# Optimization experiments

Measured on AMD Instinct MI355X. Metric: run time of the kernel, lower is better.

The kernel has to match this reference:

```python
import jax, jax.numpy as jnp
import numpy as np

H = 2048          # hidden_size
I = 8192          # intermediate_size (shared expert)
E = 32            # num_experts
K = 4             # num_experts_per_tok
M = 1408          # moe_intermediate_size
B, S = 2, 1024


def setup_inputs() -> dict:
    key = jax.random.key(0)
    ks = jax.random.split(key, 7)
    scale = 0.02
    return {
        "hidden_states": jax.random.normal(ks[0], (B, S, H), dtype=jnp.float32),
        "gate_w": jax.random.normal(ks[1], (H, E), dtype=jnp.float32) * scale,
        "w1": jax.random.normal(ks[2], (E, H, M), dtype=jnp.float32) * scale,  # expert up-proj
        "w2": jax.random.normal(ks[3], (E, M, H), dtype=jnp.float32) * scale,  # expert down-proj
        "ws1": jax.random.normal(ks[4], (H, I), dtype=jnp.float32) * scale,    # shared up-proj
        "ws2": jax.random.normal(ks[5], (I, H), dtype=jnp.float32) * scale,    # shared down-proj
    }


def reference(hidden_states, gate_w, w1, w2, ws1, ws2):
    b, s, h = hidden_states.shape
    x = hidden_states.reshape(-1, h)                      # [T, H]

    # shared expert: Linear -> SiLU -> Linear
    shared = jax.nn.silu(x @ ws1) @ ws2                   # [T, H]

    # router: top-k logits, softmax over the k selected logits
    router_logits = x @ gate_w                            # [T, E]
    top_vals, top_idx = jax.lax.top_k(router_logits, K)   # [T, K]
    routing_weights = jax.nn.softmax(top_vals, axis=-1)   # [T, K]

    # combine weights: scatter top-k weights into dense [T, E]
    cw = (jax.nn.one_hot(top_idx, E, dtype=x.dtype)
          * routing_weights[..., None]).sum(axis=1)       # [T, E]

    # expert FFNs (dense over experts, weighted combine)
    a = jax.nn.silu(jnp.einsum('th,ehm->tem', x, w1))     # [T, E, M]
    expert_out = jnp.einsum('tem,emh,te->th', a, w2, cw)  # [T, H]

    output = (shared + expert_out).reshape(b, s, h)
    return output, router_logits.reshape(b, s, E)
```

## Files before the change

kernel.cpp:

```cpp
#include <hip/hip_runtime.h>

#define H_ 2048
#define E_ 32
#define KSEL 4
#define M_ 1408
#define I_ 8192
#define T_ 2048

typedef __bf16 bf16;
typedef bf16 bf16x8 __attribute__((ext_vector_type(8)));
typedef float f32x4 __attribute__((ext_vector_type(4)));
typedef unsigned short u16x8 __attribute__((ext_vector_type(8)));
typedef unsigned int u32x4 __attribute__((ext_vector_type(4)));

static __device__ __forceinline__ unsigned short bfb(float f) {
  return __builtin_bit_cast(unsigned short, (bf16)f);
}

static __device__ __forceinline__ void gload_lds16(const void* g, void* l) {
  __builtin_amdgcn_global_load_lds((const __attribute__((address_space(1))) void*)g,
                                   (__attribute__((address_space(3))) void*)l, 16, 0, 0);
}

static __device__ __forceinline__ float silu_f(float v) {
  return v / (1.f + __expf(-v));
}

static __device__ __forceinline__ void wave_argmax(float& v, int& vi) {
  #pragma unroll
  for (int off = 32; off >= 1; off >>= 1) {
    float ov = __shfl_xor(v, off);
    int   oi = __shfl_xor(vi, off);
    if (ov > v || (ov == v && oi < vi)) { v = ov; vi = oi; }
  }
}

__global__ __launch_bounds__(64) void prep_k(int* __restrict__ counts) {
  if (threadIdx.x < E_) counts[threadIdx.x] = 0;
}

__global__ __launch_bounds__(256) void combine_k(const float* __restrict__ sc,
                                                 const float* __restrict__ sc2,
                                                 float* __restrict__ out) {
  size_t i = ((size_t)blockIdx.x * 256 + threadIdx.x) * 4;
  int t = (int)(i >> 11);
  int h = (int)(i & 2047);
  const float* s = sc + (size_t)(t * 4) * H_ + h;
  float4 a = *(const float4*)(s);
  float4 b = *(const float4*)(s + H_);
  float4 c = *(const float4*)(s + 2 * H_);
  float4 d = *(const float4*)(s + 3 * H_);
  float4 o;
  o.x = a.x + b.x + c.x + d.x;
  o.y = a.y + b.y + c.y + d.y;
  o.z = a.z + b.z + c.z + d.z;
  o.w = a.w + b.w + c.w + d.w;
  #pragma unroll
  for (int kz = 0; kz < 2; ++kz) {
    float4 v = *(const float4*)(sc2 + (size_t)kz * T_ * H_ + i);
    o.x += v.x; o.y += v.y; o.z += v.z; o.w += v.w;
  }
  *(float4*)(out + i) = o;
}

__global__ __launch_bounds__(64) void router_k(const float* __restrict__ x, const float* __restrict__ gw,
                                               float* __restrict__ logits, int* __restrict__ counts,
                                               int* __restrict__ tlist, float* __restrict__ wlist,
                                               unsigned short* __restrict__ xb) {
  int t = blockIdx.x;
  int l = threadIdx.x;

  {
    const float* xrow = x + (size_t)t * H_;
    unsigned short* xbrow = xb + (size_t)t * H_;
    #pragma unroll
    for (int j = 0; j < 4; ++j) {
      int base = j * 512 + l * 8;
      float4 a = *(const float4*)(xrow + base);
      float4 b = *(const float4*)(xrow + base + 4);
      u16x8 o;
      o[0]=bfb(a.x); o[1]=bfb(a.y); o[2]=bfb(a.z); o[3]=bfb(a.w);
      o[4]=bfb(b.x); o[5]=bfb(b.y); o[6]=bfb(b.z); o[7]=bfb(b.w);
      *(u16x8*)(xbrow + base) = o;
    }
  }

  int e = l & 31;
  int half = l >> 5;
  const float* xr = x + (size_t)t * H_ + half * (H_/2);
  const float* g  = gw + (size_t)(half * (H_/2)) * E_ + e;
  float a0=0.f, a1=0.f, a2=0.f, a3=0.f;
  for (int h = 0; h < H_/2; h += 4) {
    a0 = fmaf(xr[h],   g[(size_t)h*E_],     a0);
    a1 = fmaf(xr[h+1], g[(size_t)(h+1)*E_], a1);
    a2 = fmaf(xr[h+2], g[(size_t)(h+2)*E_], a2);
    a3 = fmaf(xr[h+3], g[(size_t)(h+3)*E_], a3);
  }
  float acc = (a0+a1)+(a2+a3);
  acc += __shfl_xor(acc, 32);
  if (l < E_) logits[(size_t)t*E_ + l] = acc;

  float cur = (l < E_) ? acc : -INFINITY;
  int myidx = (l < E_) ? e : 1000;
  float tv0,tv1,tv2,tv3; int ti0,ti1,ti2,ti3;
  { float v=cur; int vi=myidx; wave_argmax(v,vi); tv0=v; ti0=vi; if (myidx==vi) cur=-INFINITY; }
  { float v=cur; int vi=myidx; wave_argmax(v,vi); tv1=v; ti1=vi; if (myidx==vi) cur=-INFINITY; }
  { float v=cur; int vi=myidx; wave_argmax(v,vi); tv2=v; ti2=vi; if (myidx==vi) cur=-INFINITY; }
  { float v=cur; int vi=myidx; wave_argmax(v,vi); tv3=v; ti3=vi; }
  float w0 = 1.f;
  float w1 = __expf(tv1 - tv0);
  float w2 = __expf(tv2 - tv0);
  float w3 = __expf(tv3 - tv0);
  float inv = 1.f / (w0+w1+w2+w3);
  if (l < KSEL) {
    float myw = ((l==0)?w0:(l==1)?w1:(l==2)?w2:w3) * inv;
    int   myi = ((l==0)?ti0:(l==1)?ti1:(l==2)?ti2:ti3);
    int pos = atomicAdd(&counts[myi], 1);
    tlist[myi*T_ + pos] = (t << 2) | l;
    wlist[myi*T_ + pos] = myw;
  }
}

template<int MODE, int KDIM, int NDIM, int ASTR, int KSPLIT>
__device__ __forceinline__ void gemm_body(
    char* __restrict__ smem, int mt, int nt, int kz, int nrows,
    const bf16* __restrict__ A, const float* __restrict__ Bp,
    bf16* __restrict__ Cb, float* __restrict__ Cf,
    const int* __restrict__ lst, const float* __restrict__ wl)
{
  char* As = smem;
  char* Bs = smem + 16384;
  const int tid = threadIdx.x;
  const int mrow0 = mt*128, ncol0 = nt*64;

  const bf16* abase[4];
  int aoffs[4];
  #pragma unroll
  for (int c = 0; c < 4; ++c) {
    int lidx = c*256 + tid;
    int row  = lidx >> 3;
    int slot = lidx & 7;
    aoffs[c] = (slot ^ (row & 7)) * 8;
    int ri = mrow0 + row;
    if constexpr (MODE == 2) {
      int tt = (ri < nrows) ? (lst[ri] >> 2) : 0;
      abase[c] = A + (size_t)tt * ASTR;
    } else if constexpr (MODE == 3) {
      int ar = (ri < nrows) ? lst[ri] : 0;
      abase[c] = A + (size_t)ar * ASTR;
    } else {
      abase[c] = A + (size_t)ri * ASTR;
    }
  }

  const int bn = tid & 63;
  const int bq = tid >> 6;
  const float* bsrc0 = Bp + (size_t)(bq * 16) * NDIM + ncol0 + bn;
  char* const bdst = Bs + (bq*2)*1024 + bn*16;

  const int l  = tid & 63;
  const int wv = tid >> 6;
  const int wr = wv >> 1, wc = wv & 1;
  const int ss = l >> 4;

  f32x4 acc[4][2] = {};

  constexpr int ITERS = KDIM / 64 / KSPLIT;
  static_assert(ITERS % 2 == 0, "K-loop is 2-unrolled");
  const int kt0 = kz * ITERS;
  const int ktend = kt0 + ITERS;

  float vA[16], vB[16];

#define LOADB(P, KT) do {                                            \
    const float* bs_ = bsrc0 + (size_t)((KT) * 64) * NDIM;           \
    _Pragma("unroll")                                                \
    for (int j = 0; j < 16; ++j) P[j] = bs_[(size_t)j * NDIM];       \
  } while (0)

#define WRITEB(P) do {                                               \
    u32x4 lo_, hi_;                                                  \
    _Pragma("unroll")                                                \
    for (int j = 0; j < 4; ++j) {                                    \
      lo_[j] = (unsigned)bfb(P[2*j])   | ((unsigned)bfb(P[2*j+1]) << 16); \
      hi_[j] = (unsigned)bfb(P[8+2*j]) | ((unsigned)bfb(P[8+2*j+1]) << 16); \
    }                                                                \
    *(u32x4*)(bdst)        = lo_;                                    \
    *(u32x4*)(bdst + 1024) = hi_;                                    \
  } while (0)

#define MFMA_HALF(S) do {                                            \
    bf16x8 af[4], bfr[2];                                            \
    const int ks = (S)*4 + ss;                                       \
    _Pragma("unroll")                                                \
    for (int mf = 0; mf < 4; ++mf) {                                 \
      int r = wr*64 + mf*16 + (l & 15);                              \
      af[mf] = *(const bf16x8*)(As + r*128 + ((ks ^ (r & 7)) << 4)); \
    }                                                                \
    _Pragma("unroll")                                                \
    for (int nf = 0; nf < 2; ++nf) {                                 \
      int c = wc*32 + nf*16 + (l & 15);                              \
      bfr[nf] = *(const bf16x8*)(Bs + ks*1024 + c*16);               \
    }                                                                \
    _Pragma("unroll")                                                \
    for (int mf = 0; mf < 4; ++mf)                                   \
      _Pragma("unroll")                                              \
      for (int nf = 0; nf < 2; ++nf)                                 \
        acc[mf][nf] = __builtin_amdgcn_mfma_f32_16x16x32_bf16(af[mf], bfr[nf], acc[mf][nf], 0, 0, 0); \
  } while (0)

#define MFMA_PHASE() do { MFMA_HALF(0); MFMA_HALF(1); } while (0)

#define ADMA(KT) do {                                                \
    _Pragma("unroll")                                                \
    for (int c = 0; c < 4; ++c)                                      \
      gload_lds16(abase[c] + (KT)*64 + aoffs[c], As + (c*256 + tid)*16); \
  } while (0)

  LOADB(vA, kt0);
  for (int kt = kt0; kt < ktend; kt += 2) {
    __syncthreads();
    ADMA(kt);
    WRITEB(vA);
    __syncthreads();
    LOADB(vB, kt + 1);
    MFMA_PHASE();

    __syncthreads();
    ADMA(kt + 1);
    WRITEB(vB);
    __syncthreads();
    if (kt + 2 < ktend) LOADB(vA, kt + 2);
    MFMA_PHASE();
  }

#undef LOADB
#undef WRITEB
#undef MFMA_HALF
#undef MFMA_PHASE
#undef ADMA

  #pragma unroll
  for (int mf = 0; mf < 4; ++mf) {
    #pragma unroll
    for (int j = 0; j < 4; ++j) {
      const int rloc = wr*64 + mf*16 + (l >> 4)*4 + j;
      const int grow = mrow0 + rloc;
      if constexpr (MODE == 0) {
        #pragma unroll
        for (int nf = 0; nf < 2; ++nf) {
          int col = ncol0 + wc*32 + nf*16 + (l & 15);
          Cb[(size_t)grow * NDIM + col] = (bf16)silu_f(acc[mf][nf][j]);
        }
      } else if constexpr (MODE == 1) {
        float* dst = Cf + (size_t)kz * T_ * H_;
        #pragma unroll
        for (int nf = 0; nf < 2; ++nf) {
          int col = ncol0 + wc*32 + nf*16 + (l & 15);
          dst[(size_t)grow * NDIM + col] = acc[mf][nf][j];
        }
      } else if constexpr (MODE == 2) {
        if (grow < nrows) {
          int entry = lst[grow];
          float wg = wl[grow];
          #pragma unroll
          for (int nf = 0; nf < 2; ++nf) {
            int col = ncol0 + wc*32 + nf*16 + (l & 15);
            Cb[(size_t)entry * NDIM + col] = (bf16)(silu_f(acc[mf][nf][j]) * wg);
          }
        }
      } else {
        if (grow < nrows) {
          int entry = lst[grow];
          #pragma unroll
          for (int nf = 0; nf < 2; ++nf) {
            int col = ncol0 + wc*32 + nf*16 + (l & 15);
            Cf[(size_t)entry * H_ + col] = acc[mf][nf][j];
          }
        }
      }
    }
  }
}

__global__ __launch_bounds__(256) void fusedA_k(
    const bf16* __restrict__ xb, const float* __restrict__ w1, const float* __restrict__ ws1,
    bf16* __restrict__ act, bf16* __restrict__ y1,
    const int* __restrict__ tlist, const float* __restrict__ wlist, const int* __restrict__ counts)
{
  __shared__ __align__(16) char smem[24576];
  if (blockIdx.x < 1408) {
    constexpr int NT = M_ / 64;
    constexpr int NWG = NT * E_ * 2;
    constexpr int CPX = NWG / 8;
    int id = blockIdx.x;
    int lg = (id & 7) * CPX + (id >> 3);
    int bit = lg & 1;
    int en  = lg >> 1;
    int e  = en / NT;
    int nt = en % NT;
    int mt = (blockIdx.y == 0) ? bit : (2 + 2*((int)blockIdx.y - 1) + bit);
    int nrows = counts[e];
    if (mt * 128 >= nrows) return;
    gemm_body<2, 2048, M_, 2048, 1>(smem, mt, nt, 0, nrows,
        xb, w1 + (size_t)e * 2048 * M_, act, nullptr, tlist + e*T_, wlist + e*T_);
  } else {
    int t = ((int)blockIdx.x - 1408) * 8 + (int)blockIdx.y;
    constexpr int CPX = 2048 / 8;
    int lg = (t & 7) * CPX + (t >> 3);
    int mt = lg & 15;
    int nt = lg >> 4;
    gemm_body<0, 2048, I_, 2048, 1>(smem, mt, nt, 0, T_,
        xb, ws1, y1, nullptr, nullptr, nullptr);
  }
}

__global__ __launch_bounds__(256) void fusedB_k(
    const bf16* __restrict__ y1, const float* __restrict__ ws2,
    const bf16* __restrict__ act, const float* __restrict__ w2,
    float* __restrict__ scratch2, float* __restrict__ scratch,
    const int* __restrict__ tlist, const int* __restrict__ counts)
{
  __shared__ __align__(16) char smem[24576];
  if (blockIdx.x < 2048) {
    constexpr int NT = H_ / 64;
    constexpr int NWG = NT * E_ * 2;
    constexpr int CPX = NWG / 8;
    int id = blockIdx.x;
    int lg = (id & 7) * CPX + (id >> 3);
    int bit = lg & 1;
    int en  = lg >> 1;
    int e  = en / NT;
    int nt = en % NT;
    int mt = (blockIdx.y == 0) ? bit : (2 + 2*((int)blockIdx.y - 1) + bit);
    int nrows = counts[e];
    if (mt * 128 >= nrows) return;
    gemm_body<3, M_, H_, M_, 1>(smem, mt, nt, 0, nrows,
        act, w2 + (size_t)e * M_ * H_, nullptr, scratch, tlist + e*T_, nullptr);
  } else {
    int id = ((int)blockIdx.x - 2048) * 8 + (int)blockIdx.y;
    int kz  = id & 1;
    int sub = id >> 1;
    constexpr int CPX = 512 / 8;
    int lg = (sub & 7) * CPX + (sub >> 3);
    int mt = lg & 15;
    int nt = lg >> 4;
    gemm_body<1, I_, H_, I_, 2>(smem, mt, nt, kz, T_,
        y1, ws2, nullptr, scratch2, nullptr, nullptr);
  }
}

extern "C" void kernel_launch(void* const* d_in, const int* in_sizes, int n_in,
                              void* d_out, int out_size, void* d_ws, size_t ws_size,
                              hipStream_t stream) {
  const float* x   = (const float*)d_in[0];
  const float* gw  = (const float*)d_in[1];
  const float* w1  = (const float*)d_in[2];
  const float* w2  = (const float*)d_in[3];
  const float* ws1 = (const float*)d_in[4];
  const float* ws2 = (const float*)d_in[5];
  float* out    = (float*)d_out;
  float* logits = out + (size_t)T_ * H_;

  char* ws = (char*)d_ws;
  const size_t off_xb   = 0;
  const size_t off_y1   = off_xb  + (size_t)T_ * H_ * 2;
  const size_t off_act  = off_y1  + (size_t)T_ * I_ * 2;
  const size_t off_cnt  = off_act + (size_t)T_ * 4 * M_ * 2;
  const size_t off_tl   = off_cnt + 256;
  const size_t off_wl   = off_tl  + (size_t)E_ * T_ * 4;
  const size_t off_sc   = off_wl  + (size_t)E_ * T_ * 4;
  const size_t off_sc2  = off_sc  + (size_t)T_ * 4 * H_ * 4;

  const bf16* xb = (const bf16*)(ws + off_xb);
  bf16* y1  = (bf16*)(ws + off_y1);
  bf16* act = (bf16*)(ws + off_act);
  int*  counts = (int*)(ws + off_cnt);
  int*  tlist  = (int*)(ws + off_tl);
  float* wlist = (float*)(ws + off_wl);
  float* scratch  = (float*)(ws + off_sc);
  float* scratch2 = (float*)(ws + off_sc2);

  prep_k<<<1, 64, 0, stream>>>(counts);
  router_k<<<T_, 64, 0, stream>>>(x, gw, logits, counts, tlist, wlist,
                                  (unsigned short*)(ws + off_xb));

  fusedA_k<<<dim3(1408 + 256, 8), 256, 0, stream>>>(
      xb, w1, ws1, act, y1, tlist, wlist, counts);
  fusedB_k<<<dim3(2048 + 128, 8), 256, 0, stream>>>(
      y1, ws2, act, w2, scratch2, scratch, tlist, counts);
  combine_k<<<4096, 256, 0, stream>>>(scratch, scratch2, out);
}
```

Measured before the change: 750.2 us.

## Pre-transpose shared expert weights to bf16 and stream B tiles via LDS DMA

Adds a transpose-and-convert kernel that turns the fp32 shared-expert weights ws1 and ws2 into K-contiguous bf16 copies inside each call. The shared GEMM paths then load B with direct global-to-LDS DMA in a swizzled layout, the same way A is loaded, instead of fp32 register loads followed by conversion and LDS stores. The K loop for these paths is simplified to single-stage. The cost is two extra kernels per call that read 128 MB of fp32 and write 64 MB of bf16, and the loss of the register prefetch that overlapped B loads with MFMA work.

```diff
diff --git a/kernel.cpp b/kernel.cpp
--- a/kernel.cpp
+++ b/kernel.cpp
@@ -37,6 +37,31 @@
 
 __global__ __launch_bounds__(64) void prep_k(int* __restrict__ counts) {
   if (threadIdx.x < E_) counts[threadIdx.x] = 0;
+}
+
+__global__ __launch_bounds__(256) void tconv_k(const float* __restrict__ src, bf16* __restrict__ dst,
+                                               int K, int N) {
+  __shared__ bf16 lt[64][66];
+  const int t = threadIdx.x;
+  const int k0 = blockIdx.x * 64, n0 = blockIdx.y * 64;
+  #pragma unroll
+  for (int p = 0; p < 4; ++p) {
+    int r = p * 16 + (t >> 4);
+    int c = (t & 15) * 4;
+    float4 v = *(const float4*)(src + (size_t)(k0 + r) * N + n0 + c);
+    lt[c+0][r] = (bf16)v.x; lt[c+1][r] = (bf16)v.y;
+    lt[c+2][r] = (bf16)v.z; lt[c+3][r] = (bf16)v.w;
+  }
+  __syncthreads();
+  #pragma unroll
+  for (int q = 0; q < 2; ++q) {
+    int n  = q * 32 + (t >> 3);
+    int ks = (t & 7) * 8;
+    bf16x8 o;
+    #pragma unroll
+    for (int j = 0; j < 8; ++j) o[j] = lt[n][ks + j];
+    *(bf16x8*)(dst + (size_t)(n0 + n) * K + k0 + ks) = o;
+  }
 }
 
 __global__ __launch_bounds__(256) void combine_k(const float* __restrict__ sc,
@@ -124,7 +149,7 @@
 template<int MODE, int KDIM, int NDIM, int ASTR, int KSPLIT>
 __device__ __forceinline__ void gemm_body(
     char* __restrict__ smem, int mt, int nt, int kz, int nrows,
-    const bf16* __restrict__ A, const float* __restrict__ Bp,
+    const bf16* __restrict__ A, const float* __restrict__ Bp, const bf16* __restrict__ Btp,
     bf16* __restrict__ Cb, float* __restrict__ Cf,
     const int* __restrict__ lst, const float* __restrict__ wl)
 {
@@ -153,6 +178,19 @@
     }
   }
 
+  const bf16* bbaseB[2];
+  int boffs[2];
+  if constexpr (MODE <= 1) {
+    #pragma unroll
+    for (int c = 0; c < 2; ++c) {
+      int lidx = c*256 + tid;
+      int row  = lidx >> 3;
+      int slot = lidx & 7;
+      boffs[c] = (slot ^ (row & 7)) * 8;
+      bbaseB[c] = Btp + (size_t)(ncol0 + row) * KDIM;
+    }
+  }
+
   const int bn = tid & 63;
   const int bq = tid >> 6;
   const float* bsrc0 = Bp + (size_t)(bq * 16) * NDIM + ncol0 + bn;
@@ -200,7 +238,10 @@
     _Pragma("unroll")                                                \
     for (int nf = 0; nf < 2; ++nf) {                                 \
       int c = wc*32 + nf*16 + (l & 15);                              \
-      bfr[nf] = *(const bf16x8*)(Bs + ks*1024 + c*16);               \
+      if constexpr (MODE <= 1)                                       \
+        bfr[nf] = *(const bf16x8*)(Bs + c*128 + ((ks ^ (c & 7)) << 4)); \
+      else                                                           \
+        bfr[nf] = *(const bf16x8*)(Bs + ks*1024 + c*16);             \
     }                                                                \
     _Pragma("unroll")                                                \
     for (int mf = 0; mf < 4; ++mf)                                   \
@@ -217,21 +258,37 @@
       gload_lds16(abase[c] + (KT)*64 + aoffs[c], As + (c*256 + tid)*16); \
   } while (0)
 
-  LOADB(vA, kt0);
-  for (int kt = kt0; kt < ktend; kt += 2) {
-    __syncthreads();
-    ADMA(kt);
-    WRITEB(vA);
-    __syncthreads();
-    LOADB(vB, kt + 1);
-    MFMA_PHASE();
-
-    __syncthreads();
-    ADMA(kt + 1);
-    WRITEB(vB);
-    __syncthreads();
-    if (kt + 2 < ktend) LOADB(vA, kt + 2);
-    MFMA_PHASE();
+#define BDMA(KT) do {                                                \
+    _Pragma("unroll")                                                \
+    for (int c = 0; c < 2; ++c)                                      \
+      gload_lds16(bbaseB[c] + (KT)*64 + boffs[c], Bs + (c*256 + tid)*16); \
+  } while (0)
+
+  if constexpr (MODE <= 1) {
+    for (int kt = kt0; kt < ktend; ++kt) {
+      __syncthreads();
+      ADMA(kt);
+      BDMA(kt);
+      __syncthreads();
+      MFMA_PHASE();
+    }
+  } else {
+    LOADB(vA, kt0);
+    for (int kt = kt0; kt < ktend; kt += 2) {
+      __syncthreads();
+      ADMA(kt);
+      WRITEB(vA);
+      __syncthreads();
+      LOADB(vB, kt + 1);
+      MFMA_PHASE();
+
+      __syncthreads();
+      ADMA(kt + 1);
+      WRITEB(vB);
+      __syncthreads();
+      if (kt + 2 < ktend) LOADB(vA, kt + 2);
+      MFMA_PHASE();
+    }
   }
 
 #undef LOADB
@@ -239,6 +296,7 @@
 #undef MFMA_HALF
 #undef MFMA_PHASE
 #undef ADMA
+#undef BDMA
 
   #pragma unroll
   for (int mf = 0; mf < 4; ++mf) {
@@ -284,7 +342,7 @@
 }
 
 __global__ __launch_bounds__(256) void fusedA_k(
-    const bf16* __restrict__ xb, const float* __restrict__ w1, const float* __restrict__ ws1,
+    const bf16* __restrict__ xb, const float* __restrict__ w1, const bf16* __restrict__ ws1t,
     bf16* __restrict__ act, bf16* __restrict__ y1,
     const int* __restrict__ tlist, const float* __restrict__ wlist, const int* __restrict__ counts)
 {
@@ -303,7 +361,7 @@
     int nrows = counts[e];
     if (mt * 128 >= nrows) return;
     gemm_body<2, 2048, M_, 2048, 1>(smem, mt, nt, 0, nrows,
-        xb, w1 + (size_t)e * 2048 * M_, act, nullptr, tlist + e*T_, wlist + e*T_);
+        xb, w1 + (size_t)e * 2048 * M_, nullptr, act, nullptr, tlist + e*T_, wlist + e*T_);
   } else {
     int t = ((int)blockIdx.x - 1408) * 8 + (int)blockIdx.y;
     constexpr int CPX = 2048 / 8;
@@ -311,12 +369,12 @@
     int mt = lg & 15;
     int nt = lg >> 4;
     gemm_body<0, 2048, I_, 2048, 1>(smem, mt, nt, 0, T_,
-        xb, ws1, y1, nullptr, nullptr, nullptr);
+        xb, nullptr, ws1t, y1, nullptr, nullptr, nullptr);
   }
 }
 
 __global__ __launch_bounds__(256) void fusedB_k(
-    const bf16* __restrict__ y1, const float* __restrict__ ws2,
+    const bf16* __restrict__ y1, const bf16* __restrict__ ws2t,
     const bf16* __restrict__ act, const float* __restrict__ w2,
     float* __restrict__ scratch2, float* __restrict__ scratch,
     const int* __restrict__ tlist, const int* __restrict__ counts)
@@ -336,7 +394,7 @@
     int nrows = counts[e];
     if (mt * 128 >= nrows) return;
     gemm_body<3, M_, H_, M_, 1>(smem, mt, nt, 0, nrows,
-        act, w2 + (size_t)e * M_ * H_, nullptr, scratch, tlist + e*T_, nullptr);
+        act, w2 + (size_t)e * M_ * H_, nullptr, nullptr, scratch, tlist + e*T_, nullptr);
   } else {
     int id = ((int)blockIdx.x - 2048) * 8 + (int)blockIdx.y;
     int kz  = id & 1;
@@ -346,7 +404,7 @@
     int mt = lg & 15;
     int nt = lg >> 4;
     gemm_body<1, I_, H_, I_, 2>(smem, mt, nt, kz, T_,
-        y1, ws2, nullptr, scratch2, nullptr, nullptr);
+        y1, nullptr, ws2t, nullptr, scratch2, nullptr, nullptr);
   }
 }
 
@@ -371,6 +429,8 @@
   const size_t off_wl   = off_tl  + (size_t)E_ * T_ * 4;
   const size_t off_sc   = off_wl  + (size_t)E_ * T_ * 4;
   const size_t off_sc2  = off_sc  + (size_t)T_ * 4 * H_ * 4;
+  const size_t off_w1t  = off_sc2 + (size_t)2 * T_ * H_ * 4;
+  const size_t off_w2t  = off_w1t + (size_t)I_ * H_ * 2;
 
   const bf16* xb = (const bf16*)(ws + off_xb);
   bf16* y1  = (bf16*)(ws + off_y1);
@@ -380,14 +440,18 @@
   float* wlist = (float*)(ws + off_wl);
   float* scratch  = (float*)(ws + off_sc);
   float* scratch2 = (float*)(ws + off_sc2);
+  bf16* ws1t = (bf16*)(ws + off_w1t);
+  bf16* ws2t = (bf16*)(ws + off_w2t);
 
   prep_k<<<1, 64, 0, stream>>>(counts);
+  tconv_k<<<dim3(H_/64, I_/64), 256, 0, stream>>>(ws1, ws1t, H_, I_);
+  tconv_k<<<dim3(I_/64, H_/64), 256, 0, stream>>>(ws2, ws2t, I_, H_);
   router_k<<<T_, 64, 0, stream>>>(x, gw, logits, counts, tlist, wlist,
                                   (unsigned short*)(ws + off_xb));
 
   fusedA_k<<<dim3(1408 + 256, 8), 256, 0, stream>>>(
-      xb, w1, ws1, act, y1, tlist, wlist, counts);
+      xb, w1, ws1t, act, y1, tlist, wlist, counts);
   fusedB_k<<<dim3(2048 + 128, 8), 256, 0, stream>>>(
-      y1, ws2, act, w2, scratch2, scratch, tlist, counts);
+      y1, ws2t, act, w2, scratch2, scratch, tlist, counts);
   combine_k<<<4096, 256, 0, stream>>>(scratch, scratch2, out);
 }
```

Measured after the change: 721.2 us. -3.9%, faster.
